# Kernel optimization log

Measured on AMD Instinct MI355X. Metric: run time of the kernel, lower is better.

The kernel has to match this reference:

```python
import jax, jax.numpy as jnp
import numpy as np

BS = 4  # gating blocksize


def setup_inputs() -> dict:
    key = jax.random.key(0)
    k1, k2, k3 = jax.random.split(key, 3)
    batch, rows, width, cols = 8, 2048, 4096, 4096
    X = jax.random.normal(k1, (batch, rows, width), dtype=jnp.float32)
    W = jax.random.normal(k2, (width, cols), dtype=jnp.float32)
    G = jax.random.normal(k3, (batch, width // BS, cols // BS), dtype=jnp.float32)
    return {"X": X, "W": W, "G": G}


def _gmm(X, W, G):
    # Y[b,r,c] = sum_k X[b,r,k] * W[k,c] * G[b, k//BS, c//BS]
    b = X.shape[0]
    # expand block gates to elementwise resolution
    Gf = jnp.repeat(jnp.repeat(G, BS, axis=1), BS, axis=2)  # (b, width, cols)
    # per-batch gated weight, then batched GEMM
    return jnp.einsum('brk,kc,bkc->brc', X, W, Gf)


def reference(X, W, G):
    Y = _gmm(X, W, G)
    s = Y.sum()
    return s * s
```

## Files before the change

kernel.cpp:

```cpp
#include <hip/hip_runtime.h>

#define BATCH 8
#define ROWS  2048
#define WIDTH 4096
#define COLS  4096
#define KB    1024
#define CB    1024
#define RCH   32

typedef float f32x4 __attribute__((ext_vector_type(4)));

__global__ __launch_bounds__(256) void colsum_kernel(const f32x4* __restrict__ X,
                                                     float* __restrict__ xs) {
    const int k4 = blockIdx.x * 256 + threadIdx.x;
    const int b  = blockIdx.y;
    const int r0 = blockIdx.z * RCH;

    const f32x4* p = X + (size_t)(b * ROWS + r0) * (WIDTH / 4) + k4;
    float ax = 0.f, ay = 0.f, az = 0.f, aw = 0.f;
#pragma unroll 8
    for (int r = 0; r < RCH; ++r) {
        f32x4 v = p[(size_t)r * (WIDTH / 4)];
        ax += v.x; ay += v.y; az += v.z; aw += v.w;
    }
    float* dst = xs + (size_t)b * WIDTH + 4 * k4;
    atomicAdd(dst + 0, ax);
    atomicAdd(dst + 1, ay);
    atomicAdd(dst + 2, az);
    atomicAdd(dst + 3, aw);
}

__global__ __launch_bounds__(256) void gated_kernel(const f32x4* __restrict__ Wv,
                                                    const f32x4* __restrict__ Gv,
                                                    const float* __restrict__ xs,
                                                    float* __restrict__ blocksum) {
    const int t  = threadIdx.x;
    const int kb = blockIdx.x;

    f32x4 w[4][4];
#pragma unroll
    for (int j = 0; j < 4; ++j)
#pragma unroll
        for (int m = 0; m < 4; ++m)
            w[j][m] = Wv[(size_t)(4 * kb + j) * CB + 4 * t + m];

    f32x4 g[8];
#pragma unroll
    for (int b = 0; b < 8; ++b)
        g[b] = Gv[((size_t)b * KB + kb) * (CB / 4) + t];

    float w4[4][4];
#pragma unroll
    for (int j = 0; j < 4; ++j)
#pragma unroll
        for (int m = 0; m < 4; ++m)
            w4[j][m] = (w[j][m].x + w[j][m].y) + (w[j][m].z + w[j][m].w);

    float acc = 0.f;
#pragma unroll
    for (int b = 0; b < 8; ++b) {
        float xv[4];
#pragma unroll
        for (int j = 0; j < 4; ++j)
            xv[j] = xs[b * WIDTH + 4 * kb + j];
        float in0 = 0.f, in1 = 0.f, in2 = 0.f, in3 = 0.f;
#pragma unroll
        for (int j = 0; j < 4; ++j) {
            in0 += xv[j] * w4[j][0];
            in1 += xv[j] * w4[j][1];
            in2 += xv[j] * w4[j][2];
            in3 += xv[j] * w4[j][3];
        }
        acc += g[b].x * in0 + g[b].y * in1 + g[b].z * in2 + g[b].w * in3;
    }

#pragma unroll
    for (int o = 1; o < 64; o <<= 1) acc += __shfl_xor(acc, o, 64);
    __shared__ float lds[4];
    const int lane = t & 63, wid = t >> 6;
    if (lane == 0) lds[wid] = acc;
    __syncthreads();
    if (t == 0) blocksum[kb] = (lds[0] + lds[1]) + (lds[2] + lds[3]);
}

__global__ __launch_bounds__(256) void final_kernel(const f32x4* __restrict__ bs4,
                                                    float* __restrict__ out) {
    f32x4 v = bs4[threadIdx.x];
    float acc = (v.x + v.y) + (v.z + v.w);
    __shared__ float red[256];
    red[threadIdx.x] = acc;
    __syncthreads();
    for (int o = 128; o > 0; o >>= 1) {
        if (threadIdx.x < o) red[threadIdx.x] += red[threadIdx.x + o];
        __syncthreads();
    }
    if (threadIdx.x == 0) {
        float s = red[0];
        out[0] = s * s;
    }
}

extern "C" void kernel_launch(void* const* d_in, const int* in_sizes, int n_in,
                              void* d_out, int out_size, void* d_ws, size_t ws_size,
                              hipStream_t stream) {
    const float* X = (const float*)d_in[0];
    const float* W = (const float*)d_in[1];
    const float* G = (const float*)d_in[2];
    float* out = (float*)d_out;

    float* xs       = (float*)d_ws;
    float* blocksum = xs + BATCH * WIDTH;

    hipMemsetAsync(xs, 0, (size_t)BATCH * WIDTH * sizeof(float), stream);

    dim3 g1(WIDTH / 4 / 256, BATCH, ROWS / RCH);
    colsum_kernel<<<g1, 256, 0, stream>>>((const f32x4*)X, xs);

    gated_kernel<<<KB, 256, 0, stream>>>((const f32x4*)W, (const f32x4*)G, xs, blocksum);

    final_kernel<<<1, 256, 0, stream>>>((const f32x4*)blocksum, out);
}
```

Before: 90.13 us.

## Replace atomic column-sum accumulation with per-chunk partials reduced in gated kernel

The column-sum kernel now writes one f32x4 partial per (row-chunk, batch, column group) to workspace instead of doing float atomicAdds into a zeroed buffer. The memset is removed and the row chunk grows to 64 rows, giving 32 partitions. The gated kernel reduces the 32 partials for its column block with shuffles and LDS before the main computation. This removes atomic contention and the memset launch, at the cost of a larger workspace and extra partial reads plus a block sync in the gated kernel.

```diff
diff --git a/kernel.cpp b/kernel.cpp
--- a/kernel.cpp
+++ b/kernel.cpp
@@ -5,49 +5,64 @@
 #define WIDTH 4096
 #define COLS  4096
 #define KB    1024
-#define CB    1024
-#define RCH   32
+#define CBV   1024
+#define ZPART 32
+#define RCH   64
 
 typedef float f32x4 __attribute__((ext_vector_type(4)));
 
 __global__ __launch_bounds__(256) void colsum_kernel(const f32x4* __restrict__ X,
-                                                     float* __restrict__ xs) {
+                                                     f32x4* __restrict__ part) {
     const int k4 = blockIdx.x * 256 + threadIdx.x;
     const int b  = blockIdx.y;
-    const int r0 = blockIdx.z * RCH;
+    const int z  = blockIdx.z;
 
-    const f32x4* p = X + (size_t)(b * ROWS + r0) * (WIDTH / 4) + k4;
-    float ax = 0.f, ay = 0.f, az = 0.f, aw = 0.f;
+    const f32x4* p = X + (size_t)(b * ROWS + z * RCH) * (WIDTH / 4) + k4;
+    f32x4 a = {0.f, 0.f, 0.f, 0.f};
 #pragma unroll 8
     for (int r = 0; r < RCH; ++r) {
         f32x4 v = p[(size_t)r * (WIDTH / 4)];
-        ax += v.x; ay += v.y; az += v.z; aw += v.w;
+        a.x += v.x; a.y += v.y; a.z += v.z; a.w += v.w;
     }
-    float* dst = xs + (size_t)b * WIDTH + 4 * k4;
-    atomicAdd(dst + 0, ax);
-    atomicAdd(dst + 1, ay);
-    atomicAdd(dst + 2, az);
-    atomicAdd(dst + 3, aw);
+    part[((size_t)(z * BATCH + b) << 10) + k4] = a;
 }
 
 __global__ __launch_bounds__(256) void gated_kernel(const f32x4* __restrict__ Wv,
                                                     const f32x4* __restrict__ Gv,
-                                                    const float* __restrict__ xs,
+                                                    const f32x4* __restrict__ part,
                                                     float* __restrict__ blocksum) {
     const int t  = threadIdx.x;
     const int kb = blockIdx.x;
+    const int lane = t & 63, wv = t >> 6;
+
+    f32x4 v = part[((size_t)((t >> 3) * BATCH + (t & 7)) << 10) + kb];
 
     f32x4 w[4][4];
 #pragma unroll
     for (int j = 0; j < 4; ++j)
 #pragma unroll
         for (int m = 0; m < 4; ++m)
-            w[j][m] = Wv[(size_t)(4 * kb + j) * CB + 4 * t + m];
+            w[j][m] = Wv[(size_t)(4 * kb + j) * CBV + 4 * t + m];
 
     f32x4 g[8];
 #pragma unroll
     for (int b = 0; b < 8; ++b)
-        g[b] = Gv[((size_t)b * KB + kb) * (CB / 4) + t];
+        g[b] = Gv[((size_t)(b * KB + kb) << 8) + t];
+
+#pragma unroll
+    for (int o = 8; o < 64; o <<= 1) {
+        v.x += __shfl_xor(v.x, o, 64);
+        v.y += __shfl_xor(v.y, o, 64);
+        v.z += __shfl_xor(v.z, o, 64);
+        v.w += __shfl_xor(v.w, o, 64);
+    }
+    __shared__ f32x4 ldsx[4][8];
+    if (lane < 8) ldsx[wv][lane] = v;
+    __syncthreads();
+    f32x4 xs4[8];
+#pragma unroll
+    for (int b = 0; b < 8; ++b)
+        xs4[b] = (ldsx[0][b] + ldsx[1][b]) + (ldsx[2][b] + ldsx[3][b]);
 
     float w4[4][4];
 #pragma unroll
@@ -59,28 +74,25 @@
     float acc = 0.f;
 #pragma unroll
     for (int b = 0; b < 8; ++b) {
-        float xv[4];
-#pragma unroll
-        for (int j = 0; j < 4; ++j)
-            xv[j] = xs[b * WIDTH + 4 * kb + j];
         float in0 = 0.f, in1 = 0.f, in2 = 0.f, in3 = 0.f;
 #pragma unroll
         for (int j = 0; j < 4; ++j) {
-            in0 += xv[j] * w4[j][0];
-            in1 += xv[j] * w4[j][1];
-            in2 += xv[j] * w4[j][2];
-            in3 += xv[j] * w4[j][3];
+            const float xv = (j == 0) ? xs4[b].x : (j == 1) ? xs4[b].y
+                                                 : (j == 2) ? xs4[b].z : xs4[b].w;
+            in0 += xv * w4[j][0];
+            in1 += xv * w4[j][1];
+            in2 += xv * w4[j][2];
+            in3 += xv * w4[j][3];
         }
         acc += g[b].x * in0 + g[b].y * in1 + g[b].z * in2 + g[b].w * in3;
     }
 
 #pragma unroll
     for (int o = 1; o < 64; o <<= 1) acc += __shfl_xor(acc, o, 64);
-    __shared__ float lds[4];
-    const int lane = t & 63, wid = t >> 6;
-    if (lane == 0) lds[wid] = acc;
+    __shared__ float ldss[4];
+    if (lane == 0) ldss[wv] = acc;
     __syncthreads();
-    if (t == 0) blocksum[kb] = (lds[0] + lds[1]) + (lds[2] + lds[3]);
+    if (t == 0) blocksum[kb] = (ldss[0] + ldss[1]) + (ldss[2] + ldss[3]);
 }
 
 __global__ __launch_bounds__(256) void final_kernel(const f32x4* __restrict__ bs4,
@@ -108,15 +120,14 @@
     const float* G = (const float*)d_in[2];
     float* out = (float*)d_out;
 
-    float* xs       = (float*)d_ws;
-    float* blocksum = xs + BATCH * WIDTH;
+    float* part     = (float*)d_ws;
+    float* blocksum = part + (size_t)ZPART * BATCH * WIDTH;
 
-    hipMemsetAsync(xs, 0, (size_t)BATCH * WIDTH * sizeof(float), stream);
+    dim3 g1(WIDTH / 4 / 256, BATCH, ZPART);
+    colsum_kernel<<<g1, 256, 0, stream>>>((const f32x4*)X, (f32x4*)part);
 
-    dim3 g1(WIDTH / 4 / 256, BATCH, ROWS / RCH);
-    colsum_kernel<<<g1, 256, 0, stream>>>((const f32x4*)X, xs);
-
-    gated_kernel<<<KB, 256, 0, stream>>>((const f32x4*)W, (const f32x4*)G, xs, blocksum);
+    gated_kernel<<<KB, 256, 0, stream>>>((const f32x4*)W, (const f32x4*)G,
+                                         (const f32x4*)part, blocksum);
 
     final_kernel<<<1, 256, 0, stream>>>((const f32x4*)blocksum, out);
 }
```

Result: faster. 81.83 us (-9.2%).
